# Kernel tuning notes

Hardware: AMD Instinct MI355X
Metric: run time of the kernel (lower is better)

## Reference

```python
import jax, jax.numpy as jnp
import numpy as np

EPS_NORM = 1e-12  # torch F.normalize clamp_min eps
EPS_LOG = 1e-10


def setup_inputs() -> dict:
    key = jax.random.key(0)
    k1, k2 = jax.random.split(key)
    N, D = 12288, 128
    embeddings = jax.random.uniform(k1, (N, D), dtype=jnp.float32)
    adj = jax.random.uniform(k2, (N, N), dtype=jnp.float32)
    lambda_reg = jnp.float32(1.0)
    return {"embeddings": embeddings, "adj": adj, "lambda_reg": lambda_reg}


def reference(embeddings, adj, lambda_reg):
    # F.normalize(embeddings, dim=1, p=4): x / max(||x||_4, eps)
    norm4 = jnp.power(jnp.sum(jnp.abs(embeddings) ** 4, axis=1, keepdims=True), 0.25)
    e = embeddings / jnp.maximum(norm4, EPS_NORM)          # [N, D]
    log_p = jnp.log(e + EPS_LOG)                           # [N, D]
    p_log_p = jnp.sum(e * log_p, axis=1)                   # [N]
    cross = e @ log_p.T                                    # [N, N]
    kl = p_log_p[:, None] - cross                          # [N, N]
    # F.normalize(adj, p=1, dim=1): row-wise L1 normalization
    adj_n = adj / jnp.maximum(jnp.sum(jnp.abs(adj), axis=1, keepdims=True), EPS_NORM)
    return lambda_reg * jnp.sum(kl * adj_n)
```

## Files before the change

kernel.cpp:

```cpp
#include <hip/hip_runtime.h>
#include <hip/hip_bf16.h>

#define EPSN 1e-12f
#define EPSL 1e-10f
#define KSPLIT 16
#define KS 64

typedef __attribute__((ext_vector_type(8))) short short8;
typedef __attribute__((ext_vector_type(4))) float f32x4;

__device__ __forceinline__ unsigned short f2bf_rne(float f) {
  union { float f; unsigned u; } x; x.f = f;
  unsigned r = x.u + 0x7FFFu + ((x.u >> 16) & 1u);
  return (unsigned short)(r >> 16);
}

__global__ __launch_bounds__(256)
void prep_kernel(const float* __restrict__ emb, float* __restrict__ e,
                 unsigned short* __restrict__ lpB, float* __restrict__ plp,
                 float* __restrict__ S, float* __restrict__ v, int N) {
  int w = threadIdx.x >> 6, l = threadIdx.x & 63;
  int row = blockIdx.x * 4 + w;
  if (row >= N) return;
  const float* x = emb + (size_t)row * 128;
  float2 xv = *(const float2*)(x + 2 * l);
  float s4 = xv.x*xv.x*xv.x*xv.x + xv.y*xv.y*xv.y*xv.y;
  #pragma unroll
  for (int m = 1; m < 64; m <<= 1) s4 += __shfl_xor(s4, m);
  float denom = fmaxf(sqrtf(sqrtf(s4)), EPSN);
  float e0 = xv.x / denom, e1 = xv.y / denom;
  float lp0 = logf(e0 + EPSL), lp1 = logf(e1 + EPSL);
  e[(size_t)row * 128 + 2*l]     = e0;
  e[(size_t)row * 128 + 2*l + 1] = e1;
  int ksr = row >> 5, lhir = (row >> 3) & 3, jr = row & 7;
  int d0 = 2 * l, d1 = 2 * l + 1;
  lpB[((size_t)(ksr*8 + (d0>>4))*64 + (d0&15) + 16*lhir)*8 + jr] = f2bf_rne(lp0);
  lpB[((size_t)(ksr*8 + (d1>>4))*64 + (d1&15) + 16*lhir)*8 + jr] = f2bf_rne(lp1);
  float pl = e0 * lp0 + e1 * lp1;
  #pragma unroll
  for (int m = 1; m < 64; m <<= 1) pl += __shfl_xor(pl, m);
  if (l == 0) { plp[row] = pl; S[row] = 0.f; v[row] = 0.f; }
}

__global__ __launch_bounds__(256, 2)
void gemm_kernel(const float* __restrict__ adj, const float* __restrict__ e,
                 const unsigned short* __restrict__ lpB,
                 float* __restrict__ S, float* __restrict__ v, int N) {
  __shared__ unsigned short bsh[2][KS * 128];
  int w = threadIdx.x >> 6, l = threadIdx.x & 63;
  int l16 = l & 15, lhi = l >> 4;
  int wrow0 = blockIdx.x * 128 + w * 32;
  int kr = N / KSPLIT;
  int k0 = blockIdx.y * kr;
  int nt = kr / KS;

  f32x4 acc[2][8];
  #pragma unroll
  for (int i = 0; i < 2; ++i)
    #pragma unroll
    for (int j = 0; j < 8; ++j) acc[i][j] = (f32x4){0.f, 0.f, 0.f, 0.f};
  float sAcc[2] = {0.f, 0.f};

  const float* rp0 = adj + (size_t)(wrow0 + l16) * N + k0 + lhi * 8;
  const float* rp1 = rp0 + (size_t)16 * N;

  float4 aset0[2][2][2], aset1[2][2][2];
  float4 rB0[4], rB1[4];

#define LOADA(buf, t)                                                   \
  {                                                                     \
    _Pragma("unroll")                                                   \
    for (int rt_ = 0; rt_ < 2; ++rt_) {                                 \
      const float* bp_ = (rt_ ? rp1 : rp0) + (t) * KS;                  \
      _Pragma("unroll")                                                 \
      for (int ks_ = 0; ks_ < 2; ++ks_) {                               \
        buf[rt_][ks_][0] = *(const float4*)(bp_ + ks_ * 32);            \
        buf[rt_][ks_][1] = *(const float4*)(bp_ + ks_ * 32 + 4);        \
      }                                                                 \
    }                                                                   \
  }

#define LOADB(dst, t)                                                   \
  {                                                                     \
    const char* p_ = (const char*)lpB + (((size_t)(k0 + (t) * KS)) << 8) \
                     + w * 4096 + l * 16;                               \
    _Pragma("unroll")                                                   \
    for (int i_ = 0; i_ < 4; ++i_)                                      \
      dst[i_] = *(const float4*)(p_ + i_ * 1024);                       \
  }

#define WRITEB(bi, src)                                                 \
  {                                                                     \
    char* q_ = (char*)bsh[bi] + w * 4096 + l * 16;                      \
    _Pragma("unroll")                                                   \
    for (int i_ = 0; i_ < 4; ++i_)                                      \
      *(float4*)(q_ + i_ * 1024) = src[i_];                             \
  }

#define STEP(abuf, bi)                                                  \
  {                                                                     \
    _Pragma("unroll")                                                   \
    for (int ks_ = 0; ks_ < 2; ++ks_) {                                 \
      short8 bb_[8];                                                    \
      _Pragma("unroll")                                                 \
      for (int ct_ = 0; ct_ < 8; ++ct_)                                 \
        bb_[ct_] = *(const short8*)((char*)bsh[bi] + (ks_*8 + ct_)*1024 + l*16); \
      short8 af_[2];                                                    \
      _Pragma("unroll")                                                 \
      for (int rt_ = 0; rt_ < 2; ++rt_) {                               \
        float4 x0_ = abuf[rt_][ks_][0], x1_ = abuf[rt_][ks_][1];        \
        sAcc[rt_] += ((x0_.x + x0_.y) + (x0_.z + x0_.w)) +              \
                     ((x1_.x + x1_.y) + (x1_.z + x1_.w));               \
        short8 t_;                                                      \
        t_[0] = (short)f2bf_rne(x0_.x); t_[1] = (short)f2bf_rne(x0_.y); \
        t_[2] = (short)f2bf_rne(x0_.z); t_[3] = (short)f2bf_rne(x0_.w); \
        t_[4] = (short)f2bf_rne(x1_.x); t_[5] = (short)f2bf_rne(x1_.y); \
        t_[6] = (short)f2bf_rne(x1_.z); t_[7] = (short)f2bf_rne(x1_.w); \
        af_[rt_] = t_;                                                  \
      }                                                                 \
      __builtin_amdgcn_s_setprio(1);                                    \
      _Pragma("unroll")                                                 \
      for (int ct_ = 0; ct_ < 8; ++ct_) {                               \
        acc[0][ct_] = __builtin_amdgcn_mfma_f32_16x16x32_bf16(af_[0], bb_[ct_], acc[0][ct_], 0, 0, 0); \
        acc[1][ct_] = __builtin_amdgcn_mfma_f32_16x16x32_bf16(af_[1], bb_[ct_], acc[1][ct_], 0, 0, 0); \
      }                                                                 \
      __builtin_amdgcn_s_setprio(0);                                    \
    }                                                                   \
  }

#define FENCE_BARRIER()                                                 \
  {                                                                     \
    asm volatile("s_waitcnt lgkmcnt(0)" ::: "memory");                  \
    __builtin_amdgcn_s_barrier();                                       \
    asm volatile("" ::: "memory");                                      \
  }

  LOADB(rB0, 0);
  LOADA(aset0, 0);
  LOADB(rB1, 1);
  LOADA(aset1, 1);
  WRITEB(0, rB0);
  FENCE_BARRIER();

  for (int t = 0; t < nt; t += 2) {
    STEP(aset0, 0);
    WRITEB(1, rB1);
    if (t + 2 < nt) { LOADB(rB0, t + 2); LOADA(aset0, t + 2); }
    FENCE_BARRIER();

    STEP(aset1, 1);
    if (t + 2 < nt) WRITEB(0, rB0);
    if (t + 3 < nt) { LOADB(rB1, t + 3); LOADA(aset1, t + 3); }
    FENCE_BARRIER();
  }

  #pragma unroll
  for (int rt = 0; rt < 2; ++rt) {
    float s = sAcc[rt];
    s += __shfl_xor(s, 16);
    s += __shfl_xor(s, 32);
    if (l < 16) atomicAdd(&S[wrow0 + rt * 16 + l], s);
  }

  #pragma unroll
  for (int rt = 0; rt < 2; ++rt) {
    #pragma unroll
    for (int r = 0; r < 4; ++r) {
      int row = wrow0 + rt * 16 + lhi * 4 + r;
      float p = 0.f;
      #pragma unroll
      for (int ct = 0; ct < 8; ++ct)
        p += e[(size_t)row * 128 + ct * 16 + l16] * acc[rt][ct][r];
      p += __shfl_xor(p, 1);
      p += __shfl_xor(p, 2);
      p += __shfl_xor(p, 4);
      p += __shfl_xor(p, 8);
      if (l16 == 0) atomicAdd(&v[row], p);
    }
  }
}

__global__ __launch_bounds__(1024)
void final_kernel(const float* __restrict__ plp, const float* __restrict__ S,
                  const float* __restrict__ v, const float* __restrict__ lam,
                  float* __restrict__ out, int N) {
  __shared__ float red[16];
  float acc = 0.f;
  for (int i = threadIdx.x; i < N; i += 1024) {
    float s = S[i], d = fmaxf(s, EPSN);
    acc += plp[i] * (s / d) - v[i] / d;
  }
  #pragma unroll
  for (int m = 1; m < 64; m <<= 1) acc += __shfl_xor(acc, m);
  int w = threadIdx.x >> 6, l = threadIdx.x & 63;
  if (l == 0) red[w] = acc;
  __syncthreads();
  if (threadIdx.x == 0) {
    float t = 0.f;
    #pragma unroll
    for (int i = 0; i < 16; ++i) t += red[i];
    out[0] = lam[0] * t;
  }
}

extern "C" void kernel_launch(void* const* d_in, const int* in_sizes, int n_in,
                              void* d_out, int out_size, void* d_ws, size_t ws_size,
                              hipStream_t stream) {
  const float* emb = (const float*)d_in[0];
  const float* adj = (const float*)d_in[1];
  const float* lam = (const float*)d_in[2];
  int N = in_sizes[0] / 128;

  char* ws = (char*)d_ws;
  float* e            = (float*)ws;
  unsigned short* lpB = (unsigned short*)(ws + (size_t)N * 512);
  float* plp          = (float*)(ws + (size_t)N * 768);
  float* S            = plp + N;
  float* v            = S + N;

  prep_kernel<<<(N + 3) / 4, 256, 0, stream>>>(emb, e, lpB, plp, S, v, N);
  dim3 grid(N / 128, KSPLIT);
  gemm_kernel<<<grid, 256, 0, stream>>>(adj, e, lpB, S, v, N);
  final_kernel<<<1, 1024, 0, stream>>>(plp, S, v, lam, (float*)d_out, N);
}
```

Baseline: 247.2 us.

## Restructure GEMM pipeline with deeper B prefetch and fragment-matched e layout

Reorganizes the main loop so each iteration writes the next B tile to LDS before computing, then prefetches B three tiles ahead and A two tiles ahead. The goal is to better overlap global loads with MFMA work. It also writes normalized embeddings in a layout matching the MFMA accumulator fragments, so the epilogue uses vectorized float4 loads and batched shuffle reductions. Register pressure and ordering hazards on the reused B register set are the main risks.

```diff
diff --git a/kernel.cpp b/kernel.cpp
--- a/kernel.cpp
+++ b/kernel.cpp
@@ -16,7 +16,7 @@
 }
 
 __global__ __launch_bounds__(256)
-void prep_kernel(const float* __restrict__ emb, float* __restrict__ e,
+void prep_kernel(const float* __restrict__ emb, float* __restrict__ eC,
                  unsigned short* __restrict__ lpB, float* __restrict__ plp,
                  float* __restrict__ S, float* __restrict__ v, int N) {
   int w = threadIdx.x >> 6, l = threadIdx.x & 63;
@@ -30,10 +30,11 @@
   float denom = fmaxf(sqrtf(sqrtf(s4)), EPSN);
   float e0 = xv.x / denom, e1 = xv.y / denom;
   float lp0 = logf(e0 + EPSL), lp1 = logf(e1 + EPSL);
-  e[(size_t)row * 128 + 2*l]     = e0;
-  e[(size_t)row * 128 + 2*l + 1] = e1;
+  int Rg = row >> 4, lhig = (row >> 2) & 3, rg = row & 3;
+  int d0 = 2 * l, d1 = 2 * l + 1;
+  eC[(((size_t)Rg * 8 + (d0 >> 4)) * 64 + (d0 & 15) + 16 * lhig) * 4 + rg] = e0;
+  eC[(((size_t)Rg * 8 + (d1 >> 4)) * 64 + (d1 & 15) + 16 * lhig) * 4 + rg] = e1;
   int ksr = row >> 5, lhir = (row >> 3) & 3, jr = row & 7;
-  int d0 = 2 * l, d1 = 2 * l + 1;
   lpB[((size_t)(ksr*8 + (d0>>4))*64 + (d0&15) + 16*lhir)*8 + jr] = f2bf_rne(lp0);
   lpB[((size_t)(ksr*8 + (d1>>4))*64 + (d1&15) + 16*lhir)*8 + jr] = f2bf_rne(lp1);
   float pl = e0 * lp0 + e1 * lp1;
@@ -43,7 +44,7 @@
 }
 
 __global__ __launch_bounds__(256, 2)
-void gemm_kernel(const float* __restrict__ adj, const float* __restrict__ e,
+void gemm_kernel(const float* __restrict__ adj, const float* __restrict__ eC,
                  const unsigned short* __restrict__ lpB,
                  float* __restrict__ S, float* __restrict__ v, int N) {
   __shared__ unsigned short bsh[2][KS * 128];
@@ -135,23 +136,26 @@
     asm volatile("" ::: "memory");                                      \
   }
 
+#define ITER(t, ASET, RB, BI)                                           \
+  {                                                                     \
+    if ((t) + 1 < nt) WRITEB((BI) ^ 1, RB);                             \
+    if ((t) + 3 < nt) LOADB(RB, (t) + 3);                               \
+    STEP(ASET, BI);                                                     \
+    if ((t) + 2 < nt) LOADA(ASET, (t) + 2);                             \
+    FENCE_BARRIER();                                                    \
+  }
+
   LOADB(rB0, 0);
   LOADA(aset0, 0);
-  LOADB(rB1, 1);
   LOADA(aset1, 1);
   WRITEB(0, rB0);
+  LOADB(rB0, 1);
+  LOADB(rB1, 2);
   FENCE_BARRIER();
 
   for (int t = 0; t < nt; t += 2) {
-    STEP(aset0, 0);
-    WRITEB(1, rB1);
-    if (t + 2 < nt) { LOADB(rB0, t + 2); LOADA(aset0, t + 2); }
-    FENCE_BARRIER();
-
-    STEP(aset1, 1);
-    if (t + 2 < nt) WRITEB(0, rB0);
-    if (t + 3 < nt) { LOADB(rB1, t + 3); LOADA(aset1, t + 3); }
-    FENCE_BARRIER();
+    ITER(t,     aset0, rB0, 0);
+    ITER(t + 1, aset1, rB1, 1);
   }
 
   #pragma unroll
@@ -164,18 +168,29 @@
 
   #pragma unroll
   for (int rt = 0; rt < 2; ++rt) {
-    #pragma unroll
-    for (int r = 0; r < 4; ++r) {
-      int row = wrow0 + rt * 16 + lhi * 4 + r;
-      float p = 0.f;
-      #pragma unroll
-      for (int ct = 0; ct < 8; ++ct)
-        p += e[(size_t)row * 128 + ct * 16 + l16] * acc[rt][ct][r];
-      p += __shfl_xor(p, 1);
-      p += __shfl_xor(p, 2);
-      p += __shfl_xor(p, 4);
-      p += __shfl_xor(p, 8);
-      if (l16 == 0) atomicAdd(&v[row], p);
+    int R = (wrow0 >> 4) + rt;
+    float p0 = 0.f, p1 = 0.f, p2 = 0.f, p3 = 0.f;
+    #pragma unroll
+    for (int ct = 0; ct < 8; ++ct) {
+      float4 ef = *(const float4*)(eC + (((size_t)R * 8 + ct) * 64 + l) * 4);
+      p0 += ef.x * acc[rt][ct][0];
+      p1 += ef.y * acc[rt][ct][1];
+      p2 += ef.z * acc[rt][ct][2];
+      p3 += ef.w * acc[rt][ct][3];
+    }
+    #pragma unroll
+    for (int m = 1; m < 16; m <<= 1) {
+      p0 += __shfl_xor(p0, m);
+      p1 += __shfl_xor(p1, m);
+      p2 += __shfl_xor(p2, m);
+      p3 += __shfl_xor(p3, m);
+    }
+    if (l16 == 0) {
+      int rowb = wrow0 + rt * 16 + lhi * 4;
+      atomicAdd(&v[rowb + 0], p0);
+      atomicAdd(&v[rowb + 1], p1);
+      atomicAdd(&v[rowb + 2], p2);
+      atomicAdd(&v[rowb + 3], p3);
     }
   }
 }
@@ -212,14 +227,14 @@
   int N = in_sizes[0] / 128;
 
   char* ws = (char*)d_ws;
-  float* e            = (float*)ws;
+  float* eC           = (float*)ws;
   unsigned short* lpB = (unsigned short*)(ws + (size_t)N * 512);
   float* plp          = (float*)(ws + (size_t)N * 768);
   float* S            = plp + N;
   float* v            = S + N;
 
-  prep_kernel<<<(N + 3) / 4, 256, 0, stream>>>(emb, e, lpB, plp, S, v, N);
+  prep_kernel<<<(N + 3) / 4, 256, 0, stream>>>(emb, eC, lpB, plp, S, v, N);
   dim3 grid(N / 128, KSPLIT);
-  gemm_kernel<<<grid, 256, 0, stream>>>(adj, e, lpB, S, v, N);
+  gemm_kernel<<<grid, 256, 0, stream>>>(adj, eC, lpB, S, v, N);
   final_kernel<<<1, 1024, 0, stream>>>(plp, S, v, lam, (float*)d_out, N);
 }
```

Measured after the change: 246.2 us. No clear change (-0.4%).
